# Kernel tuning notes

Hardware: AMD Instinct MI355X
Metric: run time of the kernel (lower is better)

The kernel has to match this reference:

```python
import jax, jax.numpy as jnp
import numpy as np

EPS = 1e-5

def grid_sample_bilinear(img, grid):
    """torch F.grid_sample, mode='bilinear', padding_mode='zeros', align_corners=True.
    img: (b, c, H, W); grid: (b, Hg, Wg, 2) with (x, y) in [-1, 1]. Returns (b, c, Hg, Wg)."""
    H, W = img.shape[2], img.shape[3]
    x = (grid[..., 0] + 1.0) * 0.5 * (W - 1)
    y = (grid[..., 1] + 1.0) * 0.5 * (H - 1)
    x0 = jnp.floor(x); y0 = jnp.floor(y)
    x1 = x0 + 1.0;     y1 = y0 + 1.0
    wx1 = x - x0; wx0 = 1.0 - wx1
    wy1 = y - y0; wy0 = 1.0 - wy1

    def sample_one(img_b, yi, xi):
        # img_b: (c,H,W); yi, xi: (Hg,Wg) float corner coords
        valid = ((yi >= 0) & (yi < H) & (xi >= 0) & (xi < W)).astype(img_b.dtype)
        yc = jnp.clip(yi, 0, H - 1).astype(jnp.int32)
        xc = jnp.clip(xi, 0, W - 1).astype(jnp.int32)
        return img_b[:, yc, xc] * valid[None]  # (c,Hg,Wg)

    def per_batch(img_b, x0b, x1b, y0b, y1b, wx0b, wx1b, wy0b, wy1b):
        v = (sample_one(img_b, y0b, x0b) * (wy0b * wx0b)[None]
             + sample_one(img_b, y0b, x1b) * (wy0b * wx1b)[None]
             + sample_one(img_b, y1b, x0b) * (wy1b * wx0b)[None]
             + sample_one(img_b, y1b, x1b) * (wy1b * wx1b)[None])
        return v

    return jax.vmap(per_batch)(img, x0, x1, y0, y1, wx0, wx1, wy0, wy1)


def conv_bn_relu(x, w, gamma, beta):
    # 1x1 conv (no bias) + BatchNorm2d (batch stats, training-mode forward) + ReLU
    y = jnp.einsum('nchw,oc->nohw', x, w)
    mean = y.mean(axis=(0, 2, 3), keepdims=True)
    var = y.var(axis=(0, 2, 3), keepdims=True)
    y = (y - mean) * jax.lax.rsqrt(var + EPS)
    y = y * gamma[None, :, None, None] + beta[None, :, None, None]
    return jax.nn.relu(y)


def setup_inputs() -> dict:
    key = jax.random.key(0)
    ks = jax.random.split(key, 10)
    b, c, h, w, r = 1, 128, 64, 128, 4
    d = 2 * r + 1
    f1 = jax.random.normal(ks[0], (b, c, h, w), dtype=jnp.float32)
    f2 = jax.random.normal(ks[1], (b, c, h, w), dtype=jnp.float32)
    # coords: base pixel grid (x, y) plus a small random flow perturbation
    gy, gx = jnp.meshgrid(jnp.arange(h, dtype=jnp.float32), jnp.arange(w, dtype=jnp.float32), indexing='ij')
    base = jnp.stack([gx, gy], axis=0)[None]  # (1,2,h,w)
    coords = base + 2.0 * jax.random.normal(ks[2], (b, 2, h, w), dtype=jnp.float32)
    c1, c2, c3 = 96, 128, 64
    w1 = jax.random.normal(ks[3], (c1, 2 * c), dtype=jnp.float32) * 0.05
    w2 = jax.random.normal(ks[4], (c2, c1), dtype=jnp.float32) * 0.05
    w3 = jax.random.normal(ks[5], (c3, c2), dtype=jnp.float32) * 0.05
    w4 = jax.random.normal(ks[6], (1, c3), dtype=jnp.float32) * 0.05
    b4 = jnp.zeros((1,), dtype=jnp.float32)
    g1 = jnp.ones((c1,), jnp.float32); be1 = jnp.zeros((c1,), jnp.float32)
    g2 = jnp.ones((c2,), jnp.float32); be2 = jnp.zeros((c2,), jnp.float32)
    g3 = jnp.ones((c3,), jnp.float32); be3 = jnp.zeros((c3,), jnp.float32)
    # DAP: identity init + small noise so gradients are non-trivial
    wdap = jnp.eye(d * d, dtype=jnp.float32) + 0.01 * jax.random.normal(ks[7], (d * d, d * d), dtype=jnp.float32)
    return {"f1": f1, "f2": f2, "coords": coords,
            "w1": w1, "g1": g1, "be1": be1,
            "w2": w2, "g2": g2, "be2": be2,
            "w3": w3, "g3": g3, "be3": be3,
            "w4": w4, "b4": b4, "wdap": wdap, "radius": 4}


def reference(f1, f2, coords, w1, g1, be1, w2, g2, be2, w3, g3, be3, w4, b4, wdap, radius):
    b, c, h, w = f1.shape
    r = radius
    d = 2 * r + 1
    dx = jnp.linspace(-r, r, d, dtype=f1.dtype)
    delta = jnp.stack(jnp.meshgrid(dx, dx, indexing='ij'), axis=-1)  # (d,d,2)
    coords_p = jnp.transpose(coords, (0, 2, 3, 1))  # (b,h,w,2)
    cent = coords_p[:, None, :, None, :, :] + delta.reshape(1, d, 1, d, 1, 2)  # (b,d,h,d,w,2)
    cx = 2.0 * cent[..., 0] / (w - 1) - 1.0
    cy = 2.0 * cent[..., 1] / (h - 1) - 1.0
    grid = jnp.stack([cx, cy], axis=-1).reshape(b, d * h, d * w, 2)
    f2s = grid_sample_bilinear(f2, grid)                     # (b,c,d*h,d*w)
    f2s = f2s.reshape(b, c, d, h, d, w).transpose(0, 2, 4, 1, 3, 5)  # (b,d,d,c,h,w)
    f1e = jnp.broadcast_to(f1[:, None, None], (b, d, d, c, h, w))
    corr = jnp.concatenate([f1e, f2s], axis=3).reshape(b * d * d, 2 * c, h, w)
    x = conv_bn_relu(corr, w1, g1, be1)
    x = conv_bn_relu(x, w2, g2, be2)
    x = conv_bn_relu(x, w3, g3, be3)
    cost = jnp.einsum('nchw,oc->nohw', x, w4) + b4[None, :, None, None]  # (b*d*d,1,h,w)
    cost = cost.reshape(b, d * d, h, w)
    # DAP: 1x1 conv over the d*d displacement channels, no bias
    cost = jnp.einsum('bkhw,lk->blhw', cost, wdap)
    return cost  # (b, (2r+1)^2, h, w)
```

## Files before the change

kernel.cpp:

```cpp
#include <hip/hip_runtime.h>
#include <hip/hip_bf16.h>

#define H 64
#define W 128
#define P 8192
#define DD 81
#define NS 663552
#define C1 96
#define C2 128
#define C3 64
#define EPSF 1e-5f
#define NSLOT 128

#define X1S 104
#define X2S 136
#define X1TS 136

#define NGB 324
#define NGSLOT 8

typedef __attribute__((ext_vector_type(8))) short bf16x8;
typedef __attribute__((ext_vector_type(4))) float f32x4;

#define S1SUM 0
#define S1SSQ (S1SUM + NSLOT * C1)
#define M1SUM (S1SSQ + NSLOT * C1)
#define S3SUM (M1SUM + NSLOT * C1)
#define S3SSQ (S3SUM + NSLOT * C3)
#define GSLOT (S3SSQ + NSLOT * C3)
#define STATS_ZERO_FLOATS (GSLOT + NGSLOT * 9216)
#define S1Sc 126976
#define S1Tc (S1Sc + C1)
#define S2Sc (S1Tc + C1)
#define S2Tc (S2Sc + C2)
#define S3Sc (S2Tc + C2)
#define S3Tc (S3Sc + C3)
#define GOFF 127552
#define COST_OFF (GOFF + 9216)
#define FLOAT_END (COST_OFF + NS)
#define A_BYTE   ((size_t)FLOAT_END * 4)
#define G_BYTE   (A_BYTE + (size_t)P * 96 * 2)
#define W2BF_BYTE (G_BYTE + (size_t)P * 96 * 2)
#define W3BF_BYTE (W2BF_BYTE + (size_t)C2 * C1 * 2)
#define Y1_BYTE  (W3BF_BYTE + (size_t)C3 * C2 * 2)
#define Y3_BYTE  (Y1_BYTE + (size_t)NS * C1 * 2)
#define WS_NEEDED (Y3_BYTE + (size_t)NS * C3 * 2)

__device__ __forceinline__ float bflo(unsigned u) { return __uint_as_float(u << 16); }
__device__ __forceinline__ float bfhi(unsigned u) { return __uint_as_float(u & 0xffff0000u); }
__device__ __forceinline__ float bfu(unsigned short v) { return __uint_as_float((unsigned)v << 16); }

__device__ __forceinline__ unsigned pkbf(float a, float b) {
  __hip_bfloat162 h = __float22bfloat162_rn(make_float2(a, b));
  unsigned u; __builtin_memcpy(&u, &h, 4);
  return u;
}

__global__ __launch_bounds__(256) void k_prep(const float* __restrict__ f1,
                                              const float* __restrict__ f2,
                                              const float* __restrict__ w1,
                                              unsigned short* __restrict__ aT,
                                              unsigned short* __restrict__ gT) {
  __shared__ float tile[128][64];
  int t = threadIdx.x;
  int p0 = blockIdx.x * 64;
  int px = t & 63, q = t >> 6;
  int c0 = q * 24;
  for (int pass = 0; pass < 2; ++pass) {
    const float* src = pass ? f2 : f1;
    unsigned short* dst = pass ? gT : aT;
    int koff = pass ? 128 : 0;
    __syncthreads();
    for (int idx = t; idx < 8192; idx += 256) {
      int kk = idx >> 6, xx = idx & 63;
      tile[kk][xx] = src[kk * P + p0 + xx];
    }
    __syncthreads();
    float acc[24];
#pragma unroll
    for (int i = 0; i < 24; ++i) acc[i] = 0.f;
    for (int kk = 0; kk < 128; ++kk) {
      float fv = tile[kk][px];
#pragma unroll
      for (int i = 0; i < 24; ++i)
        acc[i] += w1[(c0 + i) * 256 + koff + kk] * fv;
    }
#pragma unroll
    for (int i = 0; i < 24; i += 4) {
      uint2 pk;
      pk.x = pkbf(acc[i + 0], acc[i + 1]);
      pk.y = pkbf(acc[i + 2], acc[i + 3]);
      *(uint2*)(dst + ((size_t)((c0 + i) >> 2) * P + p0 + px) * 4) = pk;
    }
  }
}

__global__ void k_wprep(const float* __restrict__ w2, const float* __restrict__ w3,
                        unsigned short* __restrict__ w2bf, unsigned short* __restrict__ w3bf) {
  int idx = blockIdx.x * 256 + threadIdx.x;
  if (idx < C2 * C1) {
    w2bf[idx] = (unsigned short)(pkbf(w2[idx], 0.f) & 0xffffu);
  } else if (idx < C2 * C1 + C3 * C2) {
    w3bf[idx - C2 * C1] = (unsigned short)(pkbf(w3[idx - C2 * C1], 0.f) & 0xffffu);
  }
}

__global__ __launch_bounds__(256) void k_sample(const float* __restrict__ coords,
                                                float* __restrict__ ws,
                                                const unsigned short* __restrict__ aT,
                                                const unsigned short* __restrict__ gT,
                                                unsigned short* __restrict__ y1T) {
  int t = threadIdx.x, b = blockIdx.x;
  int sub = b % 18;
  int ptile = b / 18;
  int cg = sub / 3, jt = sub % 3;
  int j0 = jt * 3;
  int c = cg * 4 + (t >> 6);
  int px = t & 63;
  int p = ptile * 64 + px;
  float cx = coords[p], cy = coords[P + p];
  float fx0 = floorf(cx), fy0 = floorf(cy);
  float wx1 = cx - fx0, wx0 = 1.f - wx1;
  float wy1 = cy - fy0, wy0 = 1.f - wy1;
  int ixb = (int)fx0 - 4 + j0, iyb = (int)fy0 - 4;
  int colOff[4];
  float vxv[4];
#pragma unroll
  for (int j = 0; j < 4; ++j) {
    int ix = ixb + j;
    vxv[j] = (ix >= 0 && ix < W) ? 1.f : 0.f;
    colOff[j] = min(max(ix, 0), W - 1);
  }
  float ewx0[3], ewx1[3];
#pragma unroll
  for (int j = 0; j < 3; ++j) { ewx0[j] = wx0 * vxv[j]; ewx1[j] = wx1 * vxv[j + 1]; }
  float av[4];
  {
    uint2 a2 = *(const uint2*)(aT + ((size_t)c * P + p) * 4);
    av[0] = bflo(a2.x); av[1] = bfhi(a2.x); av[2] = bflo(a2.y); av[3] = bfhi(a2.y);
  }
  const unsigned short* gc = gT + (size_t)c * P * 4;
  unsigned short* yb = y1T + ((size_t)c * P + p) * 4;
  float Hb[2][3][4];
  float sum[4] = {0.f, 0.f, 0.f, 0.f}, ssq[4] = {0.f, 0.f, 0.f, 0.f};
  float vyPrev = 0.f;
#pragma unroll
  for (int dy = 0; dy < 10; ++dy) {
    const int cur = dy & 1, prv = cur ^ 1;
    int iy = iyb + dy;
    float vy = (iy >= 0 && iy < H) ? 1.f : 0.f;
    const unsigned short* grow = gc + (size_t)(min(max(iy, 0), H - 1) * W) * 4;
    uint2 gv[4];
#pragma unroll
    for (int j = 0; j < 4; ++j) gv[j] = *(const uint2*)(grow + colOff[j] * 4);
#pragma unroll
    for (int j = 0; j < 3; ++j) {
      Hb[cur][j][0] = fmaf(ewx1[j], bflo(gv[j + 1].x), ewx0[j] * bflo(gv[j].x));
      Hb[cur][j][1] = fmaf(ewx1[j], bfhi(gv[j + 1].x), ewx0[j] * bfhi(gv[j].x));
      Hb[cur][j][2] = fmaf(ewx1[j], bflo(gv[j + 1].y), ewx0[j] * bflo(gv[j].y));
      Hb[cur][j][3] = fmaf(ewx1[j], bfhi(gv[j + 1].y), ewx0[j] * bfhi(gv[j].y));
    }
    if (dy >= 1) {
      const int dyk = dy - 1;
      float e0 = wy0 * vyPrev, e1 = wy1 * vy;
#pragma unroll
      for (int j = 0; j < 3; ++j) {
        float o0 = fmaf(e0, Hb[prv][j][0], fmaf(e1, Hb[cur][j][0], av[0]));
        float o1 = fmaf(e0, Hb[prv][j][1], fmaf(e1, Hb[cur][j][1], av[1]));
        float o2 = fmaf(e0, Hb[prv][j][2], fmaf(e1, Hb[cur][j][2], av[2]));
        float o3 = fmaf(e0, Hb[prv][j][3], fmaf(e1, Hb[cur][j][3], av[3]));
        sum[0] += o0; ssq[0] = fmaf(o0, o0, ssq[0]);
        sum[1] += o1; ssq[1] = fmaf(o1, o1, ssq[1]);
        sum[2] += o2; ssq[2] = fmaf(o2, o2, ssq[2]);
        sum[3] += o3; ssq[3] = fmaf(o3, o3, ssq[3]);
        uint2 pk;
        pk.x = pkbf(o0, o1);
        pk.y = pkbf(o2, o3);
        int kk = (j0 + j) * 9 + dyk;
        *(uint2*)(yb + (size_t)kk * 24 * P * 4) = pk;
      }
    }
    vyPrev = vy;
  }
#pragma unroll
  for (int m = 1; m < 64; m <<= 1) {
#pragma unroll
    for (int e = 0; e < 4; ++e) {
      sum[e] += __shfl_xor(sum[e], m);
      ssq[e] += __shfl_xor(ssq[e], m);
    }
  }
  if ((t & 63) == 0) {
    int slot = b & (NSLOT - 1);
#pragma unroll
    for (int e = 0; e < 4; ++e) {
      atomicAdd(&ws[S1SUM + slot * C1 + c * 4 + e], sum[e]);
      atomicAdd(&ws[S1SSQ + slot * C1 + c * 4 + e], ssq[e]);
    }
  }
}

__global__ void k_finalize(float* __restrict__ ws, int sumO, int ssqO,
                           const float* __restrict__ gamma, const float* __restrict__ beta,
                           int sO, int tO, int C) {
  int c = threadIdx.x;
  if (c < C) {
    float su = 0.f, sq = 0.f;
    for (int s = 0; s < NSLOT; ++s) { su += ws[sumO + s * C + c]; sq += ws[ssqO + s * C + c]; }
    float mean = su * (1.0f / (float)NS);
    float var = sq * (1.0f / (float)NS) - mean * mean;
    float sc = gamma[c] * rsqrtf(var + EPSF);
    ws[sO + c] = sc;
    ws[tO + c] = beta[c] - mean * sc;
  }
}

__global__ __launch_bounds__(256) void k_gram(const unsigned short* __restrict__ y1T,
                                              float* __restrict__ ws) {
  __shared__ unsigned short x1t[96 * X1TS];
  int t = threadIdx.x, b = blockIdx.x;
  int w = t >> 6, l = t & 63;
  int lr = l & 15, lh = l >> 4;
  int i0 = (w >> 1) * 48, j0 = (w & 1) * 48;
  f32x4 acc[9];
  f32x4 zero4 = {0.f, 0.f, 0.f, 0.f};
#pragma unroll
  for (int q = 0; q < 9; ++q) acc[q] = zero4;
  int c = t >> 3, pg = t & 7;
  float s1v[4], t1v[4];
  if (c < 24) {
#pragma unroll
    for (int e = 0; e < 4; ++e) { s1v[e] = ws[S1Sc + c * 4 + e]; t1v[e] = ws[S1Tc + c * 4 + e]; }
  }
  float msum[4] = {0.f, 0.f, 0.f, 0.f};
  for (int it = 0; it < 16; ++it) {
    int idx = b * 16 + it;
    int k = idx >> 6, p0 = (idx & 63) << 7;
    const unsigned short* y1k = y1T + (size_t)k * P * 96;
    __syncthreads();
    if (c < 24) {
      int pbase = p0 + pg * 16;
      unsigned rowu[4][8];
#pragma unroll
      for (int ii = 0; ii < 8; ++ii) {
        uint4 v = *(const uint4*)(y1k + ((size_t)c * P + pbase + ii * 2) * 4);
        float x00 = fmaxf(0.f, fmaf(s1v[0], bflo(v.x), t1v[0]));
        float x10 = fmaxf(0.f, fmaf(s1v[1], bfhi(v.x), t1v[1]));
        float x20 = fmaxf(0.f, fmaf(s1v[2], bflo(v.y), t1v[2]));
        float x30 = fmaxf(0.f, fmaf(s1v[3], bfhi(v.y), t1v[3]));
        float x01 = fmaxf(0.f, fmaf(s1v[0], bflo(v.z), t1v[0]));
        float x11 = fmaxf(0.f, fmaf(s1v[1], bfhi(v.z), t1v[1]));
        float x21 = fmaxf(0.f, fmaf(s1v[2], bflo(v.w), t1v[2]));
        float x31 = fmaxf(0.f, fmaf(s1v[3], bfhi(v.w), t1v[3]));
        msum[0] += x00 + x01; msum[1] += x10 + x11;
        msum[2] += x20 + x21; msum[3] += x30 + x31;
        rowu[0][ii] = pkbf(x00, x01);
        rowu[1][ii] = pkbf(x10, x11);
        rowu[2][ii] = pkbf(x20, x21);
        rowu[3][ii] = pkbf(x30, x31);
      }
#pragma unroll
      for (int e = 0; e < 4; ++e) {
        unsigned short* dst = x1t + (c * 4 + e) * X1TS + pg * 16;
        uint4 pk0; pk0.x = rowu[e][0]; pk0.y = rowu[e][1]; pk0.z = rowu[e][2]; pk0.w = rowu[e][3];
        uint4 pk1; pk1.x = rowu[e][4]; pk1.y = rowu[e][5]; pk1.z = rowu[e][6]; pk1.w = rowu[e][7];
        *(uint4*)dst = pk0;
        *(uint4*)(dst + 8) = pk1;
      }
    }
    __syncthreads();
#pragma unroll
    for (int kk = 0; kk < 4; ++kk) {
      bf16x8 a3[3], b3[3];
#pragma unroll
      for (int a = 0; a < 3; ++a)
        a3[a] = *(const bf16x8*)(const void*)(x1t + (i0 + a * 16 + lr) * X1TS + kk * 32 + lh * 8);
#pragma unroll
      for (int bb = 0; bb < 3; ++bb)
        b3[bb] = *(const bf16x8*)(const void*)(x1t + (j0 + bb * 16 + lr) * X1TS + kk * 32 + lh * 8);
#pragma unroll
      for (int a = 0; a < 3; ++a)
#pragma unroll
        for (int bb = 0; bb < 3; ++bb)
          acc[a * 3 + bb] = __builtin_amdgcn_mfma_f32_16x16x32_bf16(a3[a], b3[bb], acc[a * 3 + bb], 0, 0, 0);
    }
  }
  {
    float* gp = ws + GSLOT + (b & (NGSLOT - 1)) * 9216;
#pragma unroll
    for (int a = 0; a < 3; ++a)
#pragma unroll
      for (int bb = 0; bb < 3; ++bb) {
        int ti = (w >> 1) * 3 + a, tj = (w & 1) * 3 + bb;
        f32x4 v = acc[a * 3 + bb];
#pragma unroll
        for (int r = 0; r < 4; ++r)
          atomicAdd(&gp[(ti * 16 + lh * 4 + r) * 96 + tj * 16 + lr], v[r]);
      }
  }
  if (c < 24) {
#pragma unroll
    for (int m = 1; m < 8; m <<= 1)
#pragma unroll
      for (int e = 0; e < 4; ++e) msum[e] += __shfl_xor(msum[e], m);
    if (pg == 0) {
      int slot = b & (NSLOT - 1);
#pragma unroll
      for (int e = 0; e < 4; ++e) atomicAdd(&ws[M1SUM + slot * C1 + c * 4 + e], msum[e]);
    }
  }
}

__global__ void k_greduce(float* __restrict__ ws) {
  int e = blockIdx.x * 256 + threadIdx.x;
  float s = 0.f;
#pragma unroll
  for (int g = 0; g < NGSLOT; ++g) s += ws[GSLOT + g * 9216 + e];
  ws[GOFF + e] = s;
}

__global__ __launch_bounds__(256) void k_fin2g(float* __restrict__ ws,
                                               const unsigned short* __restrict__ w2bf,
                                               const float* __restrict__ g2,
                                               const float* __restrict__ be2) {
  __shared__ float wrow[96];
  __shared__ float m1f[96];
  __shared__ float red[8];
  int o = blockIdx.x, t = threadIdx.x;
  if (t < 96) {
    wrow[t] = bfu(w2bf[o * 96 + t]);
    float s = 0.f;
    for (int sl = 0; sl < NSLOT; ++sl) s += ws[M1SUM + sl * C1 + t];
    m1f[t] = s;
  }
  __syncthreads();
  float quad = 0.f;
  for (int e = t; e < 9216; e += 256) {
    int i = e / 96, j = e - i * 96;
    quad = fmaf(wrow[i] * wrow[j], ws[GOFF + e], quad);
  }
  float msm = (t < 96) ? wrow[t] * m1f[t] : 0.f;
#pragma unroll
  for (int m = 1; m < 64; m <<= 1) { quad += __shfl_xor(quad, m); msm += __shfl_xor(msm, m); }
  if ((t & 63) == 0) { red[t >> 6] = quad; red[4 + (t >> 6)] = msm; }
  __syncthreads();
  if (t == 0) {
    float q = red[0] + red[1] + red[2] + red[3];
    float mm = red[4] + red[5] + red[6] + red[7];
    float mean = mm * (1.0f / (float)NS);
    float var = q * (1.0f / (float)NS) - mean * mean;
    float sc = g2[o] * rsqrtf(var + EPSF);
    ws[S2Sc + o] = sc;
    ws[S2Tc + o] = be2[o] - mean * sc;
  }
}

__device__ __forceinline__ void build_x1(const unsigned short* __restrict__ y1k,
                                         const float* __restrict__ ws,
                                         unsigned short* lds, int p0, int t) {
  int s = t >> 1, hh = t & 1;
  int p = p0 + s;
  const float* s1p = ws + S1Sc;
  const float* t1p = ws + S1Tc;
  unsigned short* base = lds + s * X1S + hh * 48;
#pragma unroll
  for (int i2 = 0; i2 < 6; ++i2) {
    int c0 = hh * 12 + i2 * 2;
    uint2 va = *(const uint2*)(y1k + ((size_t)c0 * P + p) * 4);
    uint2 vb = *(const uint2*)(y1k + ((size_t)(c0 + 1) * P + p) * 4);
    int cb = c0 * 4;
    float x0 = fmaxf(0.f, fmaf(s1p[cb + 0], bflo(va.x), t1p[cb + 0]));
    float x1 = fmaxf(0.f, fmaf(s1p[cb + 1], bfhi(va.x), t1p[cb + 1]));
    float x2 = fmaxf(0.f, fmaf(s1p[cb + 2], bflo(va.y), t1p[cb + 2]));
    float x3 = fmaxf(0.f, fmaf(s1p[cb + 3], bfhi(va.y), t1p[cb + 3]));
    float x4 = fmaxf(0.f, fmaf(s1p[cb + 4], bflo(vb.x), t1p[cb + 4]));
    float x5 = fmaxf(0.f, fmaf(s1p[cb + 5], bfhi(vb.x), t1p[cb + 5]));
    float x6 = fmaxf(0.f, fmaf(s1p[cb + 6], bflo(vb.y), t1p[cb + 6]));
    float x7 = fmaxf(0.f, fmaf(s1p[cb + 7], bfhi(vb.y), t1p[cb + 7]));
    uint4 pk;
    pk.x = pkbf(x0, x1); pk.y = pkbf(x2, x3); pk.z = pkbf(x4, x5); pk.w = pkbf(x6, x7);
    *(uint4*)(base + i2 * 8) = pk;
  }
}

__global__ __launch_bounds__(256) void k_l23(const unsigned short* __restrict__ y1T,
                                             float* __restrict__ ws,
                                             const unsigned short* __restrict__ w2bf,
                                             const unsigned short* __restrict__ w3bf,
                                             unsigned short* __restrict__ y3T) {
  __shared__ unsigned short ldss[128 * X1S];
  int t = threadIdx.x, b = blockIdx.x;
  int k = b >> 6, p0 = (b & 63) << 7;
  size_t n0 = (size_t)k * P + p0;
  int slot = b & (NSLOT - 1);
  const unsigned short* y1k = y1T + (size_t)k * P * 96;
  build_x1(y1k, ws, ldss, p0, t);
  __syncthreads();
  int l = t & 63, wv = t >> 6;
  int o0w = wv * 32;
  int lr = l & 15, lh = l >> 4;
  bf16x8 af[2][3];
#pragma unroll
  for (int m = 0; m < 2; ++m)
#pragma unroll
    for (int kk = 0; kk < 3; ++kk)
      af[m][kk] = *(const bf16x8*)(const void*)(w2bf + (size_t)(o0w + m * 16 + lr) * 96 + kk * 32 + lh * 8);
  f32x4 acc[2][8];
  f32x4 zero4 = {0.f, 0.f, 0.f, 0.f};
#pragma unroll
  for (int m = 0; m < 2; ++m)
#pragma unroll
    for (int n = 0; n < 8; ++n) acc[m][n] = zero4;
#pragma unroll
  for (int kk = 0; kk < 3; ++kk)
#pragma unroll
    for (int n = 0; n < 8; ++n) {
      bf16x8 bfr = *(const bf16x8*)(const void*)(ldss + (n * 16 + lr) * X1S + kk * 32 + lh * 8);
      acc[0][n] = __builtin_amdgcn_mfma_f32_16x16x32_bf16(af[0][kk], bfr, acc[0][n], 0, 0, 0);
      acc[1][n] = __builtin_amdgcn_mfma_f32_16x16x32_bf16(af[1][kk], bfr, acc[1][n], 0, 0, 0);
    }
  float s2v[2][4], t2v[2][4];
#pragma unroll
  for (int m = 0; m < 2; ++m)
#pragma unroll
    for (int r = 0; r < 4; ++r) {
      int cc = o0w + m * 16 + lh * 4 + r;
      s2v[m][r] = ws[S2Sc + cc];
      t2v[m][r] = ws[S2Tc + cc];
    }
  int o2 = wv * 16;
  int ch4 = wv * 4 + lh;
  bf16x8 af2[4];
#pragma unroll
  for (int kk = 0; kk < 4; ++kk)
    af2[kk] = *(const bf16x8*)(const void*)(w3bf + (size_t)(o2 + lr) * 128 + kk * 32 + lh * 8);
  unsigned short* x2s = ldss;
  float ssum[4] = {0.f, 0.f, 0.f, 0.f}, sssq[4] = {0.f, 0.f, 0.f, 0.f};
#pragma unroll
  for (int h = 0; h < 2; ++h) {
    __syncthreads();
#pragma unroll
    for (int m = 0; m < 2; ++m)
#pragma unroll
      for (int n2 = 0; n2 < 4; ++n2) {
        f32x4 v = acc[m][h * 4 + n2];
        float x0 = fmaxf(0.f, fmaf(s2v[m][0], v[0], t2v[m][0]));
        float x1v = fmaxf(0.f, fmaf(s2v[m][1], v[1], t2v[m][1]));
        float x2v = fmaxf(0.f, fmaf(s2v[m][2], v[2], t2v[m][2]));
        float x3 = fmaxf(0.f, fmaf(s2v[m][3], v[3], t2v[m][3]));
        uint2 pk;
        pk.x = pkbf(x0, x1v);
        pk.y = pkbf(x2v, x3);
        *(uint2*)(x2s + (n2 * 16 + lr) * X2S + o0w + m * 16 + lh * 4) = pk;
      }
    __syncthreads();
    f32x4 acc2[4];
#pragma unroll
    for (int n2 = 0; n2 < 4; ++n2) acc2[n2] = zero4;
#pragma unroll
    for (int kk = 0; kk < 4; ++kk)
#pragma unroll
      for (int n2 = 0; n2 < 4; ++n2) {
        bf16x8 bfr = *(const bf16x8*)(const void*)(x2s + (n2 * 16 + lr) * X2S + kk * 32 + lh * 8);
        acc2[n2] = __builtin_amdgcn_mfma_f32_16x16x32_bf16(af2[kk], bfr, acc2[n2], 0, 0, 0);
      }
#pragma unroll
    for (int n2 = 0; n2 < 4; ++n2) {
      f32x4 v = acc2[n2];
#pragma unroll
      for (int r = 0; r < 4; ++r) { float x = v[r]; ssum[r] += x; sssq[r] = fmaf(x, x, sssq[r]); }
      uint2 pk;
      pk.x = pkbf(v[0], v[1]);
      pk.y = pkbf(v[2], v[3]);
      size_t n = n0 + h * 64 + n2 * 16 + lr;
      *(uint2*)(y3T + ((size_t)ch4 * NS + n) * 4) = pk;
    }
  }
#pragma unroll
  for (int msk = 1; msk < 16; msk <<= 1)
#pragma unroll
    for (int i = 0; i < 4; ++i) { ssum[i] += __shfl_xor(ssum[i], msk); sssq[i] += __shfl_xor(sssq[i], msk); }
  if (lr == 0) {
#pragma unroll
    for (int r = 0; r < 4; ++r) {
      int o = o2 + lh * 4 + r;
      atomicAdd(&ws[S3SUM + slot * C3 + o], ssum[r]);
      atomicAdd(&ws[S3SSQ + slot * C3 + o], sssq[r]);
    }
  }
}

__global__ __launch_bounds__(256) void k_layer4(const unsigned short* __restrict__ y3T,
                                                float* __restrict__ ws,
                                                const float* __restrict__ w4,
                                                const float* __restrict__ b4) {
  size_t n = (size_t)blockIdx.x * 256 + threadIdx.x;
  const float* s3p = ws + S3Sc;
  const float* t3p = ws + S3Tc;
  float acc = 0.f;
#pragma unroll
  for (int c16 = 0; c16 < 16; ++c16) {
    uint2 v = *(const uint2*)(y3T + ((size_t)c16 * NS + n) * 4);
    int c = c16 * 4;
    acc += fmaxf(0.f, fmaf(s3p[c + 0], bflo(v.x), t3p[c + 0])) * w4[c + 0];
    acc += fmaxf(0.f, fmaf(s3p[c + 1], bfhi(v.x), t3p[c + 1])) * w4[c + 1];
    acc += fmaxf(0.f, fmaf(s3p[c + 2], bflo(v.y), t3p[c + 2])) * w4[c + 2];
    acc += fmaxf(0.f, fmaf(s3p[c + 3], bfhi(v.y), t3p[c + 3])) * w4[c + 3];
  }
  ws[COST_OFF + n] = acc + b4[0];
}

__global__ __launch_bounds__(256) void k_dap(const float* __restrict__ ws,
                                             const float* __restrict__ wdap,
                                             float* __restrict__ out) {
  __shared__ float wd[DD * DD];
  int t = threadIdx.x;
  for (int i = t; i < DD * DD; i += 256) wd[i] = wdap[i];
  __syncthreads();
  int p = blockIdx.x * 32 + (t & 31);
  int lg = t >> 5;
  const float* cost = ws + COST_OFF;
  float cr[81];
#pragma unroll
  for (int kk = 0; kk < 81; ++kk) cr[kk] = cost[kk * P + p];
  for (int l = lg; l < 81; l += 8) {
    float acc = 0.f;
#pragma unroll
    for (int kk = 0; kk < 81; ++kk) acc = fmaf(wd[l * 81 + kk], cr[kk], acc);
    out[(size_t)l * P + p] = acc;
  }
}

__global__ void k_marker(float* out) { out[0] = 1.0e30f; }

extern "C" void kernel_launch(void* const* d_in, const int* in_sizes, int n_in,
                              void* d_out, int out_size, void* d_ws, size_t ws_size,
                              hipStream_t stream) {
  const float* f1 = (const float*)d_in[0];
  const float* f2 = (const float*)d_in[1];
  const float* coords = (const float*)d_in[2];
  const float* w1 = (const float*)d_in[3];
  const float* g1 = (const float*)d_in[4];
  const float* be1 = (const float*)d_in[5];
  const float* w2 = (const float*)d_in[6];
  const float* g2 = (const float*)d_in[7];
  const float* be2 = (const float*)d_in[8];
  const float* w3 = (const float*)d_in[9];
  const float* g3 = (const float*)d_in[10];
  const float* be3 = (const float*)d_in[11];
  const float* w4 = (const float*)d_in[12];
  const float* b4 = (const float*)d_in[13];
  const float* wdap = (const float*)d_in[14];
  float* out = (float*)d_out;
  float* ws = (float*)d_ws;

  if (ws_size < WS_NEEDED) {
    k_marker<<<1, 1, 0, stream>>>(out);
    return;
  }
  unsigned short* aT = (unsigned short*)((char*)d_ws + A_BYTE);
  unsigned short* gT = (unsigned short*)((char*)d_ws + G_BYTE);
  unsigned short* w2bf = (unsigned short*)((char*)d_ws + W2BF_BYTE);
  unsigned short* w3bf = (unsigned short*)((char*)d_ws + W3BF_BYTE);
  unsigned short* y1T = (unsigned short*)((char*)d_ws + Y1_BYTE);
  unsigned short* y3T = (unsigned short*)((char*)d_ws + Y3_BYTE);

  hipMemsetAsync(d_ws, 0, (size_t)STATS_ZERO_FLOATS * 4, stream);
  k_prep<<<128, 256, 0, stream>>>(f1, f2, w1, aT, gT);
  k_wprep<<<80, 256, 0, stream>>>(w2, w3, w2bf, w3bf);
  k_sample<<<2304, 256, 0, stream>>>(coords, ws, aT, gT, y1T);
  k_finalize<<<1, 128, 0, stream>>>(ws, S1SUM, S1SSQ, g1, be1, S1Sc, S1Tc, C1);
  k_gram<<<NGB, 256, 0, stream>>>(y1T, ws);
  k_greduce<<<36, 256, 0, stream>>>(ws);
  k_fin2g<<<128, 256, 0, stream>>>(ws, w2bf, g2, be2);
  k_l23<<<5184, 256, 0, stream>>>(y1T, ws, w2bf, w3bf, y3T);
  k_finalize<<<1, 128, 0, stream>>>(ws, S3SUM, S3SSQ, g3, be3, S3Sc, S3Tc, C3);
  k_layer4<<<2592, 256, 0, stream>>>(y3T, ws, w4, b4);
  k_dap<<<256, 256, 0, stream>>>(ws, wdap, out);
}
```

Before: 288.1 us.

## Pack intermediate channels in groups of eight and remap l23 block order

The channel-interleaved layout of aT, gT and y1T changes from 4-channel groups to 8-channel groups, so every gather and store in k_sample, k_gram and k_l23 becomes a 16-byte access instead of 8 bytes. k_sample now handles 8 channels per thread and runs half as many blocks. k_l23 also gets a swizzled block index that spreads consecutive block IDs across eight strided groups, apparently to improve cache locality across XCDs. The cost is more registers per thread in k_sample and k_gram, and less parallelism in k_sample.

```diff
diff --git a/kernel.cpp b/kernel.cpp
--- a/kernel.cpp
+++ b/kernel.cpp
@@ -86,11 +86,13 @@
         acc[i] += w1[(c0 + i) * 256 + koff + kk] * fv;
     }
 #pragma unroll
-    for (int i = 0; i < 24; i += 4) {
-      uint2 pk;
+    for (int i = 0; i < 24; i += 8) {
+      uint4 pk;
       pk.x = pkbf(acc[i + 0], acc[i + 1]);
       pk.y = pkbf(acc[i + 2], acc[i + 3]);
-      *(uint2*)(dst + ((size_t)((c0 + i) >> 2) * P + p0 + px) * 4) = pk;
+      pk.z = pkbf(acc[i + 4], acc[i + 5]);
+      pk.w = pkbf(acc[i + 6], acc[i + 7]);
+      *(uint4*)(dst + ((size_t)((c0 + i) >> 3) * P + p0 + px) * 8) = pk;
     }
   }
 }
@@ -111,11 +113,11 @@
                                                 const unsigned short* __restrict__ gT,
                                                 unsigned short* __restrict__ y1T) {
   int t = threadIdx.x, b = blockIdx.x;
-  int sub = b % 18;
-  int ptile = b / 18;
-  int cg = sub / 3, jt = sub % 3;
+  int sub = b % 9;
+  int ptile = b / 9;
+  int jt = sub / 3, cw = sub % 3;
   int j0 = jt * 3;
-  int c = cg * 4 + (t >> 6);
+  int c8 = cw * 4 + (t >> 6);
   int px = t & 63;
   int p = ptile * 64 + px;
   float cx = coords[p], cy = coords[P + p];
@@ -134,50 +136,57 @@
   float ewx0[3], ewx1[3];
 #pragma unroll
   for (int j = 0; j < 3; ++j) { ewx0[j] = wx0 * vxv[j]; ewx1[j] = wx1 * vxv[j + 1]; }
-  float av[4];
+  float av[8];
   {
-    uint2 a2 = *(const uint2*)(aT + ((size_t)c * P + p) * 4);
-    av[0] = bflo(a2.x); av[1] = bfhi(a2.x); av[2] = bflo(a2.y); av[3] = bfhi(a2.y);
-  }
-  const unsigned short* gc = gT + (size_t)c * P * 4;
-  unsigned short* yb = y1T + ((size_t)c * P + p) * 4;
-  float Hb[2][3][4];
-  float sum[4] = {0.f, 0.f, 0.f, 0.f}, ssq[4] = {0.f, 0.f, 0.f, 0.f};
+    uint4 a4 = *(const uint4*)(aT + ((size_t)c8 * P + p) * 8);
+    av[0] = bflo(a4.x); av[1] = bfhi(a4.x); av[2] = bflo(a4.y); av[3] = bfhi(a4.y);
+    av[4] = bflo(a4.z); av[5] = bfhi(a4.z); av[6] = bflo(a4.w); av[7] = bfhi(a4.w);
+  }
+  const unsigned short* gc = gT + (size_t)c8 * P * 8;
+  unsigned short* yb = y1T + ((size_t)c8 * P + p) * 8;
+  float Hb[2][3][8];
+  float sum[8] = {0.f, 0.f, 0.f, 0.f, 0.f, 0.f, 0.f, 0.f};
+  float ssq[8] = {0.f, 0.f, 0.f, 0.f, 0.f, 0.f, 0.f, 0.f};
   float vyPrev = 0.f;
 #pragma unroll
   for (int dy = 0; dy < 10; ++dy) {
     const int cur = dy & 1, prv = cur ^ 1;
     int iy = iyb + dy;
     float vy = (iy >= 0 && iy < H) ? 1.f : 0.f;
-    const unsigned short* grow = gc + (size_t)(min(max(iy, 0), H - 1) * W) * 4;
-    uint2 gv[4];
-#pragma unroll
-    for (int j = 0; j < 4; ++j) gv[j] = *(const uint2*)(grow + colOff[j] * 4);
+    const unsigned short* grow = gc + (size_t)(min(max(iy, 0), H - 1) * W) * 8;
+    uint4 gv[4];
+#pragma unroll
+    for (int j = 0; j < 4; ++j) gv[j] = *(const uint4*)(grow + colOff[j] * 8);
 #pragma unroll
     for (int j = 0; j < 3; ++j) {
       Hb[cur][j][0] = fmaf(ewx1[j], bflo(gv[j + 1].x), ewx0[j] * bflo(gv[j].x));
       Hb[cur][j][1] = fmaf(ewx1[j], bfhi(gv[j + 1].x), ewx0[j] * bfhi(gv[j].x));
       Hb[cur][j][2] = fmaf(ewx1[j], bflo(gv[j + 1].y), ewx0[j] * bflo(gv[j].y));
       Hb[cur][j][3] = fmaf(ewx1[j], bfhi(gv[j + 1].y), ewx0[j] * bfhi(gv[j].y));
+      Hb[cur][j][4] = fmaf(ewx1[j], bflo(gv[j + 1].z), ewx0[j] * bflo(gv[j].z));
+      Hb[cur][j][5] = fmaf(ewx1[j], bfhi(gv[j + 1].z), ewx0[j] * bfhi(gv[j].z));
+      Hb[cur][j][6] = fmaf(ewx1[j], bflo(gv[j + 1].w), ewx0[j] * bflo(gv[j].w));
+      Hb[cur][j][7] = fmaf(ewx1[j], bfhi(gv[j + 1].w), ewx0[j] * bfhi(gv[j].w));
     }
     if (dy >= 1) {
       const int dyk = dy - 1;
       float e0 = wy0 * vyPrev, e1 = wy1 * vy;
 #pragma unroll
       for (int j = 0; j < 3; ++j) {
-        float o0 = fmaf(e0, Hb[prv][j][0], fmaf(e1, Hb[cur][j][0], av[0]));
-        float o1 = fmaf(e0, Hb[prv][j][1], fmaf(e1, Hb[cur][j][1], av[1]));
-        float o2 = fmaf(e0, Hb[prv][j][2], fmaf(e1, Hb[cur][j][2], av[2]));
-        float o3 = fmaf(e0, Hb[prv][j][3], fmaf(e1, Hb[cur][j][3], av[3]));
-        sum[0] += o0; ssq[0] = fmaf(o0, o0, ssq[0]);
-        sum[1] += o1; ssq[1] = fmaf(o1, o1, ssq[1]);
-        sum[2] += o2; ssq[2] = fmaf(o2, o2, ssq[2]);
-        sum[3] += o3; ssq[3] = fmaf(o3, o3, ssq[3]);
-        uint2 pk;
-        pk.x = pkbf(o0, o1);
-        pk.y = pkbf(o2, o3);
+        float o[8];
+#pragma unroll
+        for (int e = 0; e < 8; ++e) {
+          o[e] = fmaf(e0, Hb[prv][j][e], fmaf(e1, Hb[cur][j][e], av[e]));
+          sum[e] += o[e];
+          ssq[e] = fmaf(o[e], o[e], ssq[e]);
+        }
+        uint4 pk;
+        pk.x = pkbf(o[0], o[1]);
+        pk.y = pkbf(o[2], o[3]);
+        pk.z = pkbf(o[4], o[5]);
+        pk.w = pkbf(o[6], o[7]);
         int kk = (j0 + j) * 9 + dyk;
-        *(uint2*)(yb + (size_t)kk * 24 * P * 4) = pk;
+        *(uint4*)(yb + (size_t)kk * 12 * P * 8) = pk;
       }
     }
     vyPrev = vy;
@@ -185,7 +194,7 @@
 #pragma unroll
   for (int m = 1; m < 64; m <<= 1) {
 #pragma unroll
-    for (int e = 0; e < 4; ++e) {
+    for (int e = 0; e < 8; ++e) {
       sum[e] += __shfl_xor(sum[e], m);
       ssq[e] += __shfl_xor(ssq[e], m);
     }
@@ -193,9 +202,9 @@
   if ((t & 63) == 0) {
     int slot = b & (NSLOT - 1);
 #pragma unroll
-    for (int e = 0; e < 4; ++e) {
-      atomicAdd(&ws[S1SUM + slot * C1 + c * 4 + e], sum[e]);
-      atomicAdd(&ws[S1SSQ + slot * C1 + c * 4 + e], ssq[e]);
+    for (int e = 0; e < 8; ++e) {
+      atomicAdd(&ws[S1SUM + slot * C1 + c8 * 8 + e], sum[e]);
+      atomicAdd(&ws[S1SSQ + slot * C1 + c8 * 8 + e], ssq[e]);
     }
   }
 }
@@ -226,46 +235,53 @@
   f32x4 zero4 = {0.f, 0.f, 0.f, 0.f};
 #pragma unroll
   for (int q = 0; q < 9; ++q) acc[q] = zero4;
-  int c = t >> 3, pg = t & 7;
-  float s1v[4], t1v[4];
-  if (c < 24) {
-#pragma unroll
-    for (int e = 0; e < 4; ++e) { s1v[e] = ws[S1Sc + c * 4 + e]; t1v[e] = ws[S1Tc + c * 4 + e]; }
-  }
-  float msum[4] = {0.f, 0.f, 0.f, 0.f};
+  int c8 = t >> 4, pg = t & 15;
+  float s1v[8], t1v[8];
+  if (c8 < 12) {
+#pragma unroll
+    for (int e = 0; e < 8; ++e) { s1v[e] = ws[S1Sc + c8 * 8 + e]; t1v[e] = ws[S1Tc + c8 * 8 + e]; }
+  }
+  float msum[8] = {0.f, 0.f, 0.f, 0.f, 0.f, 0.f, 0.f, 0.f};
   for (int it = 0; it < 16; ++it) {
     int idx = b * 16 + it;
     int k = idx >> 6, p0 = (idx & 63) << 7;
     const unsigned short* y1k = y1T + (size_t)k * P * 96;
     __syncthreads();
-    if (c < 24) {
-      int pbase = p0 + pg * 16;
-      unsigned rowu[4][8];
-#pragma unroll
-      for (int ii = 0; ii < 8; ++ii) {
-        uint4 v = *(const uint4*)(y1k + ((size_t)c * P + pbase + ii * 2) * 4);
-        float x00 = fmaxf(0.f, fmaf(s1v[0], bflo(v.x), t1v[0]));
-        float x10 = fmaxf(0.f, fmaf(s1v[1], bfhi(v.x), t1v[1]));
-        float x20 = fmaxf(0.f, fmaf(s1v[2], bflo(v.y), t1v[2]));
-        float x30 = fmaxf(0.f, fmaf(s1v[3], bfhi(v.y), t1v[3]));
-        float x01 = fmaxf(0.f, fmaf(s1v[0], bflo(v.z), t1v[0]));
-        float x11 = fmaxf(0.f, fmaf(s1v[1], bfhi(v.z), t1v[1]));
-        float x21 = fmaxf(0.f, fmaf(s1v[2], bflo(v.w), t1v[2]));
-        float x31 = fmaxf(0.f, fmaf(s1v[3], bfhi(v.w), t1v[3]));
-        msum[0] += x00 + x01; msum[1] += x10 + x11;
-        msum[2] += x20 + x21; msum[3] += x30 + x31;
-        rowu[0][ii] = pkbf(x00, x01);
-        rowu[1][ii] = pkbf(x10, x11);
-        rowu[2][ii] = pkbf(x20, x21);
-        rowu[3][ii] = pkbf(x30, x31);
+    if (c8 < 12) {
+      int pbase = p0 + pg * 8;
+      unsigned rowu[8][4];
+#pragma unroll
+      for (int ii = 0; ii < 8; ii += 2) {
+        uint4 va = *(const uint4*)(y1k + ((size_t)c8 * P + pbase + ii) * 8);
+        uint4 vb = *(const uint4*)(y1k + ((size_t)c8 * P + pbase + ii + 1) * 8);
+        float xa[8], xb[8];
+        xa[0] = fmaxf(0.f, fmaf(s1v[0], bflo(va.x), t1v[0]));
+        xa[1] = fmaxf(0.f, fmaf(s1v[1], bfhi(va.x), t1v[1]));
+        xa[2] = fmaxf(0.f, fmaf(s1v[2], bflo(va.y), t1v[2]));
+        xa[3] = fmaxf(0.f, fmaf(s1v[3], bfhi(va.y), t1v[3]));
+        xa[4] = fmaxf(0.f, fmaf(s1v[4], bflo(va.z), t1v[4]));
+        xa[5] = fmaxf(0.f, fmaf(s1v[5], bfhi(va.z), t1v[5]));
+        xa[6] = fmaxf(0.f, fmaf(s1v[6], bflo(va.w), t1v[6]));
+        xa[7] = fmaxf(0.f, fmaf(s1v[7], bfhi(va.w), t1v[7]));
+        xb[0] = fmaxf(0.f, fmaf(s1v[0], bflo(vb.x), t1v[0]));
+        xb[1] = fmaxf(0.f, fmaf(s1v[1], bfhi(vb.x), t1v[1]));
+        xb[2] = fmaxf(0.f, fmaf(s1v[2], bflo(vb.y), t1v[2]));
+        xb[3] = fmaxf(0.f, fmaf(s1v[3], bfhi(vb.y), t1v[3]));
+        xb[4] = fmaxf(0.f, fmaf(s1v[4], bflo(vb.z), t1v[4]));
+        xb[5] = fmaxf(0.f, fmaf(s1v[5], bfhi(vb.z), t1v[5]));
+        xb[6] = fmaxf(0.f, fmaf(s1v[6], bflo(vb.w), t1v[6]));
+        xb[7] = fmaxf(0.f, fmaf(s1v[7], bfhi(vb.w), t1v[7]));
+#pragma unroll
+        for (int e = 0; e < 8; ++e) {
+          msum[e] += xa[e] + xb[e];
+          rowu[e][ii >> 1] = pkbf(xa[e], xb[e]);
+        }
       }
 #pragma unroll
-      for (int e = 0; e < 4; ++e) {
-        unsigned short* dst = x1t + (c * 4 + e) * X1TS + pg * 16;
-        uint4 pk0; pk0.x = rowu[e][0]; pk0.y = rowu[e][1]; pk0.z = rowu[e][2]; pk0.w = rowu[e][3];
-        uint4 pk1; pk1.x = rowu[e][4]; pk1.y = rowu[e][5]; pk1.z = rowu[e][6]; pk1.w = rowu[e][7];
-        *(uint4*)dst = pk0;
-        *(uint4*)(dst + 8) = pk1;
+      for (int e = 0; e < 8; ++e) {
+        unsigned short* dst = x1t + (c8 * 8 + e) * X1TS + pg * 8;
+        uint4 pk; pk.x = rowu[e][0]; pk.y = rowu[e][1]; pk.z = rowu[e][2]; pk.w = rowu[e][3];
+        *(uint4*)dst = pk;
       }
     }
     __syncthreads();
@@ -298,15 +314,15 @@
           atomicAdd(&gp[(ti * 16 + lh * 4 + r) * 96 + tj * 16 + lr], v[r]);
       }
   }
-  if (c < 24) {
-#pragma unroll
-    for (int m = 1; m < 8; m <<= 1)
-#pragma unroll
-      for (int e = 0; e < 4; ++e) msum[e] += __shfl_xor(msum[e], m);
+  if (c8 < 12) {
+#pragma unroll
+    for (int m = 1; m < 16; m <<= 1)
+#pragma unroll
+      for (int e = 0; e < 8; ++e) msum[e] += __shfl_xor(msum[e], m);
     if (pg == 0) {
       int slot = b & (NSLOT - 1);
 #pragma unroll
-      for (int e = 0; e < 4; ++e) atomicAdd(&ws[M1SUM + slot * C1 + c * 4 + e], msum[e]);
+      for (int e = 0; e < 8; ++e) atomicAdd(&ws[M1SUM + slot * C1 + c8 * 8 + e], msum[e]);
     }
   }
 }
@@ -364,22 +380,21 @@
   const float* t1p = ws + S1Tc;
   unsigned short* base = lds + s * X1S + hh * 48;
 #pragma unroll
-  for (int i2 = 0; i2 < 6; ++i2) {
-    int c0 = hh * 12 + i2 * 2;
-    uint2 va = *(const uint2*)(y1k + ((size_t)c0 * P + p) * 4);
-    uint2 vb = *(const uint2*)(y1k + ((size_t)(c0 + 1) * P + p) * 4);
-    int cb = c0 * 4;
-    float x0 = fmaxf(0.f, fmaf(s1p[cb + 0], bflo(va.x), t1p[cb + 0]));
-    float x1 = fmaxf(0.f, fmaf(s1p[cb + 1], bfhi(va.x), t1p[cb + 1]));
-    float x2 = fmaxf(0.f, fmaf(s1p[cb + 2], bflo(va.y), t1p[cb + 2]));
-    float x3 = fmaxf(0.f, fmaf(s1p[cb + 3], bfhi(va.y), t1p[cb + 3]));
-    float x4 = fmaxf(0.f, fmaf(s1p[cb + 4], bflo(vb.x), t1p[cb + 4]));
-    float x5 = fmaxf(0.f, fmaf(s1p[cb + 5], bfhi(vb.x), t1p[cb + 5]));
-    float x6 = fmaxf(0.f, fmaf(s1p[cb + 6], bflo(vb.y), t1p[cb + 6]));
-    float x7 = fmaxf(0.f, fmaf(s1p[cb + 7], bfhi(vb.y), t1p[cb + 7]));
+  for (int i = 0; i < 6; ++i) {
+    int c8i = hh * 6 + i;
+    uint4 v = *(const uint4*)(y1k + ((size_t)c8i * P + p) * 8);
+    int cb = c8i * 8;
+    float x0 = fmaxf(0.f, fmaf(s1p[cb + 0], bflo(v.x), t1p[cb + 0]));
+    float x1 = fmaxf(0.f, fmaf(s1p[cb + 1], bfhi(v.x), t1p[cb + 1]));
+    float x2 = fmaxf(0.f, fmaf(s1p[cb + 2], bflo(v.y), t1p[cb + 2]));
+    float x3 = fmaxf(0.f, fmaf(s1p[cb + 3], bfhi(v.y), t1p[cb + 3]));
+    float x4 = fmaxf(0.f, fmaf(s1p[cb + 4], bflo(v.z), t1p[cb + 4]));
+    float x5 = fmaxf(0.f, fmaf(s1p[cb + 5], bfhi(v.z), t1p[cb + 5]));
+    float x6 = fmaxf(0.f, fmaf(s1p[cb + 6], bflo(v.w), t1p[cb + 6]));
+    float x7 = fmaxf(0.f, fmaf(s1p[cb + 7], bfhi(v.w), t1p[cb + 7]));
     uint4 pk;
     pk.x = pkbf(x0, x1); pk.y = pkbf(x2, x3); pk.z = pkbf(x4, x5); pk.w = pkbf(x6, x7);
-    *(uint4*)(base + i2 * 8) = pk;
+    *(uint4*)(base + i * 8) = pk;
   }
 }
 
@@ -389,7 +404,8 @@
                                              const unsigned short* __restrict__ w3bf,
                                              unsigned short* __restrict__ y3T) {
   __shared__ unsigned short ldss[128 * X1S];
-  int t = threadIdx.x, b = blockIdx.x;
+  int t = threadIdx.x;
+  int b = (blockIdx.x & 7) * 648 + (blockIdx.x >> 3);
   int k = b >> 6, p0 = (b & 63) << 7;
   size_t n0 = (size_t)k * P + p0;
   int slot = b & (NSLOT - 1);
@@ -568,7 +584,7 @@
   hipMemsetAsync(d_ws, 0, (size_t)STATS_ZERO_FLOATS * 4, stream);
   k_prep<<<128, 256, 0, stream>>>(f1, f2, w1, aT, gT);
   k_wprep<<<80, 256, 0, stream>>>(w2, w3, w2bf, w3bf);
-  k_sample<<<2304, 256, 0, stream>>>(coords, ws, aT, gT, y1T);
+  k_sample<<<1152, 256, 0, stream>>>(coords, ws, aT, gT, y1T);
   k_finalize<<<1, 128, 0, stream>>>(ws, S1SUM, S1SSQ, g1, be1, S1Sc, S1Tc, C1);
   k_gram<<<NGB, 256, 0, stream>>>(y1T, ws);
   k_greduce<<<36, 256, 0, stream>>>(ws);
```

After: 289.0 us. No clear change (+0.3%).
